# Performance work log

Hardware: AMD Instinct MI355X
Metric: run time of the kernel (lower is better)

## Reference

```python
import jax, jax.numpy as jnp
import numpy as np

N_NODES = 100000


def setup_inputs() -> dict:
    key = jax.random.key(0)
    k1, k2, k3, k4, k5 = jax.random.split(key, 5)
    dim_in, dim_out = 128, 128
    x = jax.random.normal(k1, (N_NODES, dim_in), dtype=jnp.float32)
    edge_index = jax.random.randint(k2, (2, 1600000), 0, N_NODES, dtype=jnp.int64)
    # PyG SAGEConv params: lin_l (neighbor path, with bias), lin_r (root path, no bias)
    s = 1.0 / np.sqrt(dim_in)
    W_l = jax.random.uniform(k3, (dim_in, dim_out), jnp.float32, -s, s)
    b_l = jax.random.uniform(k4, (dim_out,), jnp.float32, -s, s)
    W_r = jax.random.uniform(k5, (dim_in, dim_out), jnp.float32, -s, s)
    return {"x": x, "edge_index": edge_index, "W_l": W_l, "b_l": b_l, "W_r": W_r}


def reference(x, edge_index, W_l, b_l, W_r):
    src, dst = edge_index[0], edge_index[1]
    # mean aggregation of source features onto target nodes
    gathered = x[src]                                   # [E, d_in]
    summed = jax.ops.segment_sum(gathered, dst, num_segments=N_NODES)
    ones = jnp.ones((edge_index.shape[1],), dtype=x.dtype)
    count = jax.ops.segment_sum(ones, dst, num_segments=N_NODES)
    agg = summed / jnp.maximum(count, 1.0)[:, None]     # [N, d_in]
    # out = lin_l(agg) + lin_r(x)
    return agg @ W_l + b_l + x @ W_r
```

## Files before the change

kernel.cpp:

```cpp
#include <hip/hip_runtime.h>

#define N_NODES 100000
#define DIM 128
#define NE 1600000
#define NTILES (N_NODES / 8)
#define GEMM_BLOCKS 2048
#define CHUNK 512
#define NCHUNK ((N_NODES + CHUNK - 1) / CHUNK)
#define NBKT2 2048
#define NB64 ((N_NODES + 63) / 64)
#define NBLK_BIN 200
#define EPB (NE / NBLK_BIN)
#define BK_CAP 2048

typedef unsigned short u16;
typedef __attribute__((ext_vector_type(8))) short bf16x8;
typedef __attribute__((ext_vector_type(4))) float f32x4;

__device__ __forceinline__ float bf2f(u16 h) {
  return __uint_as_float(((unsigned int)h) << 16);
}
__device__ __forceinline__ u16 f2bf(float f) {
  unsigned int u = __float_as_uint(f);
  unsigned int lsb = (u >> 16) & 1u;
  u += 0x7fffu + lsb;
  return (u16)(u >> 16);
}


__global__ __launch_bounds__(256) void convert_k(const float* __restrict__ x,
                                                 u16* __restrict__ A) {
  int t = blockIdx.x * 256 + threadIdx.x;
  int row = t >> 5;
  int c = (t & 31) * 4;
  float4 v = *(const float4*)(x + (size_t)row * DIM + c);
  ushort4 o;
  o.x = f2bf(v.x); o.y = f2bf(v.y); o.z = f2bf(v.z); o.w = f2bf(v.w);
  *(ushort4*)(A + (size_t)row * 256 + c) = o;
}

__global__ __launch_bounds__(256) void hist2048_k(const int* __restrict__ ei,
                                                  int* __restrict__ gh) {
  __shared__ int h[NBKT2];
  for (int i = threadIdx.x; i < NBKT2; i += 256) h[i] = 0;
  __syncthreads();
  int e0 = blockIdx.x * EPB;
  for (int i = threadIdx.x; i < EPB; i += 256)
    atomicAdd(&h[ei[NE + e0 + i] >> 6], 1);
  __syncthreads();
  for (int i = threadIdx.x; i < NBKT2; i += 256)
    if (h[i]) atomicAdd(&gh[i], h[i]);
}

__global__ __launch_bounds__(1024) void scan2048_k(const int* __restrict__ gh,
                                                   int* __restrict__ base,
                                                   int* __restrict__ cur) {
  __shared__ int p[1024];
  int t = threadIdx.x;
  int a = gh[2 * t], b = gh[2 * t + 1];
  p[t] = a + b;
  __syncthreads();
  for (int off = 1; off < 1024; off <<= 1) {
    int add = (t >= off) ? p[t - off] : 0;
    __syncthreads();
    p[t] += add;
    __syncthreads();
  }
  int e0 = p[t] - (a + b);
  base[2 * t] = e0;       cur[2 * t] = e0;
  base[2 * t + 1] = e0 + a; cur[2 * t + 1] = e0 + a;
  if (t == 1023) base[NBKT2] = p[t];
}

__global__ __launch_bounds__(256) void scatter_bin_k(const int* __restrict__ ei,
                                                     int* __restrict__ cur,
                                                     int* __restrict__ binned) {
  __shared__ int h[NBKT2];
  __shared__ int bbase[NBKT2];
  for (int i = threadIdx.x; i < NBKT2; i += 256) h[i] = 0;
  __syncthreads();
  int e0 = blockIdx.x * EPB;
  for (int i = threadIdx.x; i < EPB; i += 256)
    atomicAdd(&h[ei[NE + e0 + i] >> 6], 1);
  __syncthreads();
  for (int i = threadIdx.x; i < NBKT2; i += 256) {
    int c = h[i];
    bbase[i] = c ? atomicAdd(&cur[i], c) : 0;
    h[i] = 0;
  }
  __syncthreads();
  for (int i = threadIdx.x; i < EPB; i += 256) {
    int src = ei[e0 + i];
    int dst = ei[NE + e0 + i];
    int b = dst >> 6;
    int l = atomicAdd(&h[b], 1);
    binned[bbase[b] + l] = ((dst & 63) << 17) | src;
  }
}

__global__ __launch_bounds__(256) void aggB_k(const int* __restrict__ base,
                                              const int* __restrict__ binned,
                                              u16* __restrict__ A) {
  __shared__ int srcS[BK_CAP];
  __shared__ int hist[64];
  __shared__ int off[64];
  __shared__ int cur[64];
  const int b = blockIdx.x;
  const int lo = base[b];
  int cnt = base[b + 1] - lo;
  if (cnt > BK_CAP) cnt = BK_CAP;

  if (threadIdx.x < 64) hist[threadIdx.x] = 0;
  __syncthreads();
  for (int i = threadIdx.x; i < cnt; i += 256)
    atomicAdd(&hist[binned[lo + i] >> 17], 1);
  __syncthreads();
  if (threadIdx.x < 64) off[threadIdx.x] = hist[threadIdx.x];
  __syncthreads();
  for (int st = 1; st < 64; st <<= 1) {
    int add = 0;
    if (threadIdx.x < 64 && threadIdx.x >= st) add = off[threadIdx.x - st];
    __syncthreads();
    if (threadIdx.x < 64) off[threadIdx.x] += add;
    __syncthreads();
  }
  if (threadIdx.x < 64) cur[threadIdx.x] = off[threadIdx.x] - hist[threadIdx.x];
  __syncthreads();
  for (int i = threadIdx.x; i < cnt; i += 256) {
    int rec = binned[lo + i];
    int l = atomicAdd(&cur[rec >> 17], 1);
    srcS[l] = rec & 0x1FFFF;
  }
  __syncthreads();

  const int wid = threadIdx.x >> 6;
  const int lane = threadIdx.x & 63;
  const int node0 = b * 64;
  for (int ln = wid; ln < 64; ln += 4) {
    int node = node0 + ln;
    if (node >= N_NODES) break;
    int d = hist[ln];
    int e1 = off[ln];
    int j = e1 - d;
    float ax = 0.f, ay = 0.f;
    for (; j + 4 <= e1; j += 4) {
      int s0 = srcS[j], s1 = srcS[j + 1], s2 = srcS[j + 2], s3 = srcS[j + 3];
      unsigned u0 = *(const unsigned*)(A + (size_t)s0 * 256 + lane * 2);
      unsigned u1 = *(const unsigned*)(A + (size_t)s1 * 256 + lane * 2);
      unsigned u2 = *(const unsigned*)(A + (size_t)s2 * 256 + lane * 2);
      unsigned u3 = *(const unsigned*)(A + (size_t)s3 * 256 + lane * 2);
      ax += bf2f((u16)u0) + bf2f((u16)u1) + bf2f((u16)u2) + bf2f((u16)u3);
      ay += bf2f((u16)(u0 >> 16)) + bf2f((u16)(u1 >> 16)) +
            bf2f((u16)(u2 >> 16)) + bf2f((u16)(u3 >> 16));
    }
    for (; j < e1; ++j) {
      unsigned u0 = *(const unsigned*)(A + (size_t)srcS[j] * 256 + lane * 2);
      ax += bf2f((u16)u0);
      ay += bf2f((u16)(u0 >> 16));
    }
    float scale = 1.0f / fmaxf((float)d, 1.0f);
    unsigned p = (unsigned)f2bf(ax * scale) | ((unsigned)f2bf(ay * scale) << 16);
    *(unsigned*)(A + (size_t)node * 256 + 128 + lane * 2) = p;
  }
}

__global__ __launch_bounds__(256) void wt_k(const float* __restrict__ Wl,
                                            const float* __restrict__ Wr,
                                            u16* __restrict__ Wt) {
  int n = blockIdx.x;
  int k = threadIdx.x;
  float v = (k < 128) ? Wr[(size_t)k * DIM + n] : Wl[(size_t)(k - 128) * DIM + n];
  Wt[(size_t)n * 256 + k] = f2bf(v);
}

__global__ __launch_bounds__(256) void gemm_mfma(const u16* __restrict__ A,
                                                 const u16* __restrict__ Wt,
                                                 const float* __restrict__ bias,
                                                 float* __restrict__ out) {
  const int wave = threadIdx.x >> 6;
  const int lane = threadIdx.x & 63;
  const int m = lane & 15;
  const int q = lane >> 4;
  const int n0 = wave * 32;

  bf16x8 Bf[2][8];
#pragma unroll
  for (int t = 0; t < 2; ++t) {
    const u16* bp = Wt + (size_t)(n0 + t * 16 + m) * 256 + q * 8;
#pragma unroll
    for (int s = 0; s < 8; ++s) Bf[t][s] = *(const bf16x8*)(bp + s * 32);
  }
  const float b0 = bias[n0 + m];
  const float b1 = bias[n0 + 16 + m];

  for (int rt = blockIdx.x; rt < N_NODES / 16; rt += gridDim.x) {
    const int row0 = rt * 16;
    const u16* ap = A + (size_t)(row0 + m) * 256 + q * 8;
    bf16x8 Af[8];
#pragma unroll
    for (int s = 0; s < 8; ++s) Af[s] = *(const bf16x8*)(ap + s * 32);
    f32x4 acc0 = {0.f, 0.f, 0.f, 0.f};
    f32x4 acc1 = {0.f, 0.f, 0.f, 0.f};
#pragma unroll
    for (int s = 0; s < 8; ++s) {
      acc0 = __builtin_amdgcn_mfma_f32_16x16x32_bf16(Af[s], Bf[0][s], acc0, 0, 0, 0);
      acc1 = __builtin_amdgcn_mfma_f32_16x16x32_bf16(Af[s], Bf[1][s], acc1, 0, 0, 0);
    }
    float* o = out + (size_t)(row0 + q * 4) * DIM + n0 + m;
#pragma unroll
    for (int r = 0; r < 4; ++r) {
      o[(size_t)r * DIM] = acc0[r] + b0;
      o[(size_t)r * DIM + 16] = acc1[r] + b1;
    }
  }
}

__global__ __launch_bounds__(256) void hist_k(const int* __restrict__ ei,
                                              int* __restrict__ deg) {
  int e = blockIdx.x * 256 + threadIdx.x;
  if (e < NE) atomicAdd(&deg[ei[NE + e]], 1);
}

__global__ __launch_bounds__(512) void scan_sum_k(const int* __restrict__ deg,
                                                  int* __restrict__ partials) {
  __shared__ int s[CHUNK];
  int i = blockIdx.x * CHUNK + threadIdx.x;
  s[threadIdx.x] = (i < N_NODES) ? deg[i] : 0;
  __syncthreads();
  for (int off = 256; off > 0; off >>= 1) {
    if (threadIdx.x < off) s[threadIdx.x] += s[threadIdx.x + off];
    __syncthreads();
  }
  if (threadIdx.x == 0) partials[blockIdx.x] = s[0];
}

__global__ __launch_bounds__(256) void scan_part_k(int* __restrict__ partials) {
  __shared__ int s[256];
  int t = threadIdx.x;
  int v = (t < NCHUNK) ? partials[t] : 0;
  s[t] = v;
  __syncthreads();
  for (int off = 1; off < 256; off <<= 1) {
    int add = (t >= off) ? s[t - off] : 0;
    __syncthreads();
    s[t] += add;
    __syncthreads();
  }
  if (t < NCHUNK) partials[t] = s[t] - v;
}

__global__ __launch_bounds__(512) void scan_out_k(const int* __restrict__ deg,
                                                  const int* __restrict__ partials,
                                                  int* __restrict__ offsets,
                                                  int* __restrict__ cursor) {
  __shared__ int s[CHUNK];
  int t = threadIdx.x;
  int i = blockIdx.x * CHUNK + t;
  int v = (i < N_NODES) ? deg[i] : 0;
  s[t] = v;
  __syncthreads();
  for (int off = 1; off < CHUNK; off <<= 1) {
    int add = (t >= off) ? s[t - off] : 0;
    __syncthreads();
    s[t] += add;
    __syncthreads();
  }
  if (i < N_NODES) {
    int excl = partials[blockIdx.x] + s[t] - v;
    offsets[i] = excl;
    cursor[i] = excl;
  }
  if (i == 0) offsets[N_NODES] = NE;
}

__global__ __launch_bounds__(256) void fill_k(const int* __restrict__ ei,
                                              int* __restrict__ cursor,
                                              int* __restrict__ csr) {
  int e = blockIdx.x * 256 + threadIdx.x;
  if (e < NE) {
    int dst = ei[NE + e];
    int pos = atomicAdd(&cursor[dst], 1);
    csr[pos] = ei[e];
  }
}

__global__ __launch_bounds__(256) void agg_f32_k(const int* __restrict__ offsets,
                                                 const int* __restrict__ csr,
                                                 const float* __restrict__ x,
                                                 float* __restrict__ agg) {
  int node = blockIdx.x * 4 + (threadIdx.x >> 6);
  int lane = threadIdx.x & 63;
  int beg = offsets[node], end = offsets[node + 1];
  float ax = 0.f, ay = 0.f;
  int i = beg;
  for (; i + 4 <= end; i += 4) {
    int s0 = csr[i], s1 = csr[i + 1], s2 = csr[i + 2], s3 = csr[i + 3];
    float2 v0 = *(const float2*)(x + (size_t)s0 * DIM + lane * 2);
    float2 v1 = *(const float2*)(x + (size_t)s1 * DIM + lane * 2);
    float2 v2 = *(const float2*)(x + (size_t)s2 * DIM + lane * 2);
    float2 v3 = *(const float2*)(x + (size_t)s3 * DIM + lane * 2);
    ax += v0.x + v1.x + v2.x + v3.x;
    ay += v0.y + v1.y + v2.y + v3.y;
  }
  for (; i < end; ++i) {
    float2 v0 = *(const float2*)(x + (size_t)csr[i] * DIM + lane * 2);
    ax += v0.x;
    ay += v0.y;
  }
  float scale = 1.0f / fmaxf((float)(end - beg), 1.0f);
  float2 r;
  r.x = ax * scale;
  r.y = ay * scale;
  *(float2*)(agg + (size_t)node * DIM + lane * 2) = r;
}

__global__ __launch_bounds__(256) void gemm_xw(const float* __restrict__ x,
                                               const float* __restrict__ W,
                                               const float* __restrict__ b,
                                               float* __restrict__ out) {
  __shared__ float Ws[DIM * DIM];
  for (int i = threadIdx.x; i < DIM * DIM; i += 256) Ws[i] = W[i];
  __syncthreads();
  const int c = threadIdx.x & 127;
  const int half = threadIdx.x >> 7;
  const float bias = b[c];
  for (int tile = blockIdx.x; tile < NTILES; tile += gridDim.x) {
    const int row0 = tile * 8 + half * 4;
    const float* r = x + (size_t)row0 * DIM;
    float a0 = 0.f, a1 = 0.f, a2 = 0.f, a3 = 0.f;
#pragma unroll 8
    for (int k4 = 0; k4 < 32; ++k4) {
      float4 p0 = *(const float4*)(r + 0 * DIM + k4 * 4);
      float4 p1 = *(const float4*)(r + 1 * DIM + k4 * 4);
      float4 p2 = *(const float4*)(r + 2 * DIM + k4 * 4);
      float4 p3 = *(const float4*)(r + 3 * DIM + k4 * 4);
      const float* wp = &Ws[k4 * 4 * DIM + c];
      float w0 = wp[0 * DIM], w1 = wp[1 * DIM], w2 = wp[2 * DIM], w3 = wp[3 * DIM];
      a0 += p0.x * w0 + p0.y * w1 + p0.z * w2 + p0.w * w3;
      a1 += p1.x * w0 + p1.y * w1 + p1.z * w2 + p1.w * w3;
      a2 += p2.x * w0 + p2.y * w1 + p2.z * w2 + p2.w * w3;
      a3 += p3.x * w0 + p3.y * w1 + p3.z * w2 + p3.w * w3;
    }
    out[(size_t)(row0 + 0) * DIM + c] = a0 + bias;
    out[(size_t)(row0 + 1) * DIM + c] = a1 + bias;
    out[(size_t)(row0 + 2) * DIM + c] = a2 + bias;
    out[(size_t)(row0 + 3) * DIM + c] = a3 + bias;
  }
}

__global__ __launch_bounds__(256) void gemm_aw(const float* __restrict__ agg,
                                               const float* __restrict__ W,
                                               float* __restrict__ out) {
  __shared__ float Ws[DIM * DIM];
  for (int i = threadIdx.x; i < DIM * DIM; i += 256) Ws[i] = W[i];
  __syncthreads();
  const int c = threadIdx.x & 127;
  const int half = threadIdx.x >> 7;
  for (int tile = blockIdx.x; tile < NTILES; tile += gridDim.x) {
    const int row0 = tile * 8 + half * 4;
    const float* r = agg + (size_t)row0 * DIM;
    float a0 = 0.f, a1 = 0.f, a2 = 0.f, a3 = 0.f;
#pragma unroll 8
    for (int k4 = 0; k4 < 32; ++k4) {
      float4 p0 = *(const float4*)(r + 0 * DIM + k4 * 4);
      float4 p1 = *(const float4*)(r + 1 * DIM + k4 * 4);
      float4 p2 = *(const float4*)(r + 2 * DIM + k4 * 4);
      float4 p3 = *(const float4*)(r + 3 * DIM + k4 * 4);
      const float* wp = &Ws[k4 * 4 * DIM + c];
      float w0 = wp[0 * DIM], w1 = wp[1 * DIM], w2 = wp[2 * DIM], w3 = wp[3 * DIM];
      a0 += p0.x * w0 + p0.y * w1 + p0.z * w2 + p0.w * w3;
      a1 += p1.x * w0 + p1.y * w1 + p1.z * w2 + p1.w * w3;
      a2 += p2.x * w0 + p2.y * w1 + p2.z * w2 + p2.w * w3;
      a3 += p3.x * w0 + p3.y * w1 + p3.z * w2 + p3.w * w3;
    }
    out[(size_t)(row0 + 0) * DIM + c] += a0;
    out[(size_t)(row0 + 1) * DIM + c] += a1;
    out[(size_t)(row0 + 2) * DIM + c] += a2;
    out[(size_t)(row0 + 3) * DIM + c] += a3;
  }
}

extern "C" void kernel_launch(void* const* d_in, const int* in_sizes, int n_in,
                              void* d_out, int out_size, void* d_ws, size_t ws_size,
                              hipStream_t stream) {
  const float* x  = (const float*)d_in[0];
  const int*   ei = (const int*)d_in[1];
  const float* Wl = (const float*)d_in[2];
  const float* bl = (const float*)d_in[3];
  const float* Wr = (const float*)d_in[4];
  float* out = (float*)d_out;

  u16* A        = (u16*)d_ws;
  u16* Wt       = A + (size_t)N_NODES * 256;
  int* binned   = (int*)(Wt + 128 * 256);
  int* bktHist  = binned + NE;
  int* bktBase  = bktHist + NBKT2;
  int* bktCur   = bktBase + NBKT2 + 1;
  size_t needed = (size_t)N_NODES * 512 + 65536 + (size_t)NE * 4 +
                  (NBKT2 + NBKT2 + 1 + NBKT2) * 4;

  if (ws_size >= needed) {
    hipMemsetAsync(bktHist, 0, NBKT2 * sizeof(int), stream);
    hipLaunchKernelGGL(convert_k, dim3(12500), dim3(256), 0, stream, x, A);
    hipLaunchKernelGGL(hist2048_k, dim3(NBLK_BIN), dim3(256), 0, stream, ei, bktHist);
    hipLaunchKernelGGL(scan2048_k, dim3(1), dim3(1024), 0, stream,
                       bktHist, bktBase, bktCur);
    hipLaunchKernelGGL(scatter_bin_k, dim3(NBLK_BIN), dim3(256), 0, stream,
                       ei, bktCur, binned);
    hipLaunchKernelGGL(aggB_k, dim3(NB64), dim3(256), 0, stream,
                       bktBase, binned, A);
    hipLaunchKernelGGL(wt_k, dim3(128), dim3(256), 0, stream, Wl, Wr, Wt);
    hipLaunchKernelGGL(gemm_mfma, dim3(1280), dim3(256), 0, stream,
                       A, Wt, bl, out);
  } else {
    int* deg2      = (int*)d_ws;
    int* offsets2  = deg2 + N_NODES;
    int* partials2 = offsets2 + 100004;
    int* csr2      = partials2 + 256;
    float* agg     = (float*)(csr2 + NE);
    hipMemsetAsync(deg2, 0, (size_t)N_NODES * sizeof(int), stream);
    hipLaunchKernelGGL(hist_k, dim3((NE + 255) / 256), dim3(256), 0, stream, ei, deg2);
    hipLaunchKernelGGL(scan_sum_k, dim3(NCHUNK), dim3(CHUNK), 0, stream, deg2, partials2);
    hipLaunchKernelGGL(scan_part_k, dim3(1), dim3(256), 0, stream, partials2);
    hipLaunchKernelGGL(scan_out_k, dim3(NCHUNK), dim3(CHUNK), 0, stream,
                       deg2, partials2, offsets2, deg2);
    hipLaunchKernelGGL(fill_k, dim3((NE + 255) / 256), dim3(256), 0, stream,
                       ei, deg2, csr2);
    hipLaunchKernelGGL(agg_f32_k, dim3(N_NODES / 4), dim3(256), 0, stream,
                       offsets2, csr2, x, agg);
    hipLaunchKernelGGL(gemm_xw, dim3(GEMM_BLOCKS), dim3(256), 0, stream,
                       x, Wr, bl, out);
    hipLaunchKernelGGL(gemm_aw, dim3(GEMM_BLOCKS), dim3(256), 0, stream,
                       agg, Wl, out);
  }
}
```

Before: 270.8 us.

## Fuse convert with histogram, scan with weight transpose; split A; prefetch GEMM tiles

Merges the bf16 conversion with the destination histogram and the bucket scan with the weight transpose, which removes two kernel launches. Buckets shrink to 32 nodes (4096 buckets) so there are more aggregation blocks with less shared memory each, and aggregation caches binned records in shared memory instead of reading them twice. The bf16 x copy and the aggregated features now live in two separate dense 128-wide arrays instead of one interleaved 256-wide array, which makes gathers denser. The GEMM now software-prefetches the next row tile and uses 1250 blocks. Risks: a 32-node bucket that overflows the 1024-entry cap is silently truncated, and the 12500-block fused kernel carries a 16 KB shared array in every block.

```diff
diff --git a/kernel.cpp b/kernel.cpp
--- a/kernel.cpp
+++ b/kernel.cpp
@@ -7,11 +7,11 @@
 #define GEMM_BLOCKS 2048
 #define CHUNK 512
 #define NCHUNK ((N_NODES + CHUNK - 1) / CHUNK)
-#define NBKT2 2048
-#define NB64 ((N_NODES + 63) / 64)
+#define NBKT 4096
+#define NB32 (N_NODES / 32)
 #define NBLK_BIN 200
 #define EPB (NE / NBLK_BIN)
-#define BK_CAP 2048
+#define BK_CAP 1024
 
 typedef unsigned short u16;
 typedef __attribute__((ext_vector_type(8))) short bf16x8;
@@ -28,62 +28,77 @@
 }
 
 
-__global__ __launch_bounds__(256) void convert_k(const float* __restrict__ x,
-                                                 u16* __restrict__ A) {
+__global__ __launch_bounds__(256) void convert_hist_k(const float* __restrict__ x,
+                                                      const int* __restrict__ ei,
+                                                      u16* __restrict__ Ax,
+                                                      int* __restrict__ gh) {
+  __shared__ int h[NBKT];
   int t = blockIdx.x * 256 + threadIdx.x;
   int row = t >> 5;
   int c = (t & 31) * 4;
   float4 v = *(const float4*)(x + (size_t)row * DIM + c);
   ushort4 o;
   o.x = f2bf(v.x); o.y = f2bf(v.y); o.z = f2bf(v.z); o.w = f2bf(v.w);
-  *(ushort4*)(A + (size_t)row * 256 + c) = o;
-}
-
-__global__ __launch_bounds__(256) void hist2048_k(const int* __restrict__ ei,
-                                                  int* __restrict__ gh) {
-  __shared__ int h[NBKT2];
-  for (int i = threadIdx.x; i < NBKT2; i += 256) h[i] = 0;
-  __syncthreads();
-  int e0 = blockIdx.x * EPB;
-  for (int i = threadIdx.x; i < EPB; i += 256)
-    atomicAdd(&h[ei[NE + e0 + i] >> 6], 1);
-  __syncthreads();
-  for (int i = threadIdx.x; i < NBKT2; i += 256)
-    if (h[i]) atomicAdd(&gh[i], h[i]);
-}
-
-__global__ __launch_bounds__(1024) void scan2048_k(const int* __restrict__ gh,
-                                                   int* __restrict__ base,
-                                                   int* __restrict__ cur) {
+  *(ushort4*)(Ax + (size_t)row * DIM + c) = o;
+
+  if (blockIdx.x < NBLK_BIN) {
+    for (int i = threadIdx.x; i < NBKT; i += 256) h[i] = 0;
+    __syncthreads();
+    int e0 = blockIdx.x * EPB;
+    for (int i = threadIdx.x; i < EPB; i += 256)
+      atomicAdd(&h[ei[NE + e0 + i] >> 5], 1);
+    __syncthreads();
+    for (int i = threadIdx.x; i < NBKT; i += 256)
+      if (h[i]) atomicAdd(&gh[i], h[i]);
+  }
+}
+
+__global__ __launch_bounds__(1024) void scan_wt_k(const int* __restrict__ gh,
+                                                  int* __restrict__ base,
+                                                  int* __restrict__ cur,
+                                                  const float* __restrict__ Wl,
+                                                  const float* __restrict__ Wr,
+                                                  u16* __restrict__ Wt) {
   __shared__ int p[1024];
-  int t = threadIdx.x;
-  int a = gh[2 * t], b = gh[2 * t + 1];
-  p[t] = a + b;
-  __syncthreads();
-  for (int off = 1; off < 1024; off <<= 1) {
-    int add = (t >= off) ? p[t - off] : 0;
-    __syncthreads();
-    p[t] += add;
-    __syncthreads();
-  }
-  int e0 = p[t] - (a + b);
-  base[2 * t] = e0;       cur[2 * t] = e0;
-  base[2 * t + 1] = e0 + a; cur[2 * t + 1] = e0 + a;
-  if (t == 1023) base[NBKT2] = p[t];
+  if (blockIdx.x == 0) {
+    int t = threadIdx.x;
+    int v0 = gh[4 * t], v1 = gh[4 * t + 1], v2 = gh[4 * t + 2], v3 = gh[4 * t + 3];
+    int s = v0 + v1 + v2 + v3;
+    p[t] = s;
+    __syncthreads();
+    for (int off = 1; off < 1024; off <<= 1) {
+      int add = (t >= off) ? p[t - off] : 0;
+      __syncthreads();
+      p[t] += add;
+      __syncthreads();
+    }
+    int e = p[t] - s;
+    base[4 * t] = e;              cur[4 * t] = e;
+    base[4 * t + 1] = e + v0;     cur[4 * t + 1] = e + v0;
+    base[4 * t + 2] = e + v0 + v1;     cur[4 * t + 2] = e + v0 + v1;
+    base[4 * t + 3] = e + v0 + v1 + v2; cur[4 * t + 3] = e + v0 + v1 + v2;
+    if (t == 1023) base[NBKT] = p[t];
+  } else {
+    int idx = (blockIdx.x - 1) * 1024 + threadIdx.x;
+    int n = idx >> 8;
+    int k = idx & 255;
+    float v = (k < 128) ? Wr[(size_t)k * DIM + n] : Wl[(size_t)(k - 128) * DIM + n];
+    Wt[(size_t)n * 256 + k] = f2bf(v);
+  }
 }
 
 __global__ __launch_bounds__(256) void scatter_bin_k(const int* __restrict__ ei,
                                                      int* __restrict__ cur,
                                                      int* __restrict__ binned) {
-  __shared__ int h[NBKT2];
-  __shared__ int bbase[NBKT2];
-  for (int i = threadIdx.x; i < NBKT2; i += 256) h[i] = 0;
+  __shared__ int h[NBKT];
+  __shared__ int bbase[NBKT];
+  for (int i = threadIdx.x; i < NBKT; i += 256) h[i] = 0;
   __syncthreads();
   int e0 = blockIdx.x * EPB;
   for (int i = threadIdx.x; i < EPB; i += 256)
-    atomicAdd(&h[ei[NE + e0 + i] >> 6], 1);
-  __syncthreads();
-  for (int i = threadIdx.x; i < NBKT2; i += 256) {
+    atomicAdd(&h[ei[NE + e0 + i] >> 5], 1);
+  __syncthreads();
+  for (int i = threadIdx.x; i < NBKT; i += 256) {
     int c = h[i];
     bbase[i] = c ? atomicAdd(&cur[i], c) : 0;
     h[i] = 0;
@@ -92,42 +107,47 @@
   for (int i = threadIdx.x; i < EPB; i += 256) {
     int src = ei[e0 + i];
     int dst = ei[NE + e0 + i];
-    int b = dst >> 6;
+    int b = dst >> 5;
     int l = atomicAdd(&h[b], 1);
-    binned[bbase[b] + l] = ((dst & 63) << 17) | src;
+    binned[bbase[b] + l] = ((dst & 31) << 17) | src;
   }
 }
 
 __global__ __launch_bounds__(256) void aggB_k(const int* __restrict__ base,
                                               const int* __restrict__ binned,
-                                              u16* __restrict__ A) {
+                                              const u16* __restrict__ Ax,
+                                              u16* __restrict__ Ag) {
+  __shared__ int recS[BK_CAP];
   __shared__ int srcS[BK_CAP];
-  __shared__ int hist[64];
-  __shared__ int off[64];
-  __shared__ int cur[64];
+  __shared__ int hist[32];
+  __shared__ int off[32];
+  __shared__ int cur[32];
   const int b = blockIdx.x;
   const int lo = base[b];
   int cnt = base[b + 1] - lo;
   if (cnt > BK_CAP) cnt = BK_CAP;
 
-  if (threadIdx.x < 64) hist[threadIdx.x] = 0;
-  __syncthreads();
-  for (int i = threadIdx.x; i < cnt; i += 256)
-    atomicAdd(&hist[binned[lo + i] >> 17], 1);
-  __syncthreads();
-  if (threadIdx.x < 64) off[threadIdx.x] = hist[threadIdx.x];
-  __syncthreads();
-  for (int st = 1; st < 64; st <<= 1) {
-    int add = 0;
-    if (threadIdx.x < 64 && threadIdx.x >= st) add = off[threadIdx.x - st];
-    __syncthreads();
-    if (threadIdx.x < 64) off[threadIdx.x] += add;
-    __syncthreads();
-  }
-  if (threadIdx.x < 64) cur[threadIdx.x] = off[threadIdx.x] - hist[threadIdx.x];
+  if (threadIdx.x < 32) hist[threadIdx.x] = 0;
   __syncthreads();
   for (int i = threadIdx.x; i < cnt; i += 256) {
     int rec = binned[lo + i];
+    recS[i] = rec;
+    atomicAdd(&hist[rec >> 17], 1);
+  }
+  __syncthreads();
+  if (threadIdx.x < 32) off[threadIdx.x] = hist[threadIdx.x];
+  __syncthreads();
+  for (int st = 1; st < 32; st <<= 1) {
+    int add = 0;
+    if (threadIdx.x < 32 && threadIdx.x >= st) add = off[threadIdx.x - st];
+    __syncthreads();
+    if (threadIdx.x < 32) off[threadIdx.x] += add;
+    __syncthreads();
+  }
+  if (threadIdx.x < 32) cur[threadIdx.x] = off[threadIdx.x] - hist[threadIdx.x];
+  __syncthreads();
+  for (int i = threadIdx.x; i < cnt; i += 256) {
+    int rec = recS[i];
     int l = atomicAdd(&cur[rec >> 17], 1);
     srcS[l] = rec & 0x1FFFF;
   }
@@ -135,45 +155,36 @@
 
   const int wid = threadIdx.x >> 6;
   const int lane = threadIdx.x & 63;
-  const int node0 = b * 64;
-  for (int ln = wid; ln < 64; ln += 4) {
+  const int node0 = b * 32;
+  for (int ln = wid; ln < 32; ln += 4) {
     int node = node0 + ln;
-    if (node >= N_NODES) break;
     int d = hist[ln];
     int e1 = off[ln];
     int j = e1 - d;
     float ax = 0.f, ay = 0.f;
     for (; j + 4 <= e1; j += 4) {
       int s0 = srcS[j], s1 = srcS[j + 1], s2 = srcS[j + 2], s3 = srcS[j + 3];
-      unsigned u0 = *(const unsigned*)(A + (size_t)s0 * 256 + lane * 2);
-      unsigned u1 = *(const unsigned*)(A + (size_t)s1 * 256 + lane * 2);
-      unsigned u2 = *(const unsigned*)(A + (size_t)s2 * 256 + lane * 2);
-      unsigned u3 = *(const unsigned*)(A + (size_t)s3 * 256 + lane * 2);
+      unsigned u0 = *(const unsigned*)(Ax + (size_t)s0 * DIM + lane * 2);
+      unsigned u1 = *(const unsigned*)(Ax + (size_t)s1 * DIM + lane * 2);
+      unsigned u2 = *(const unsigned*)(Ax + (size_t)s2 * DIM + lane * 2);
+      unsigned u3 = *(const unsigned*)(Ax + (size_t)s3 * DIM + lane * 2);
       ax += bf2f((u16)u0) + bf2f((u16)u1) + bf2f((u16)u2) + bf2f((u16)u3);
       ay += bf2f((u16)(u0 >> 16)) + bf2f((u16)(u1 >> 16)) +
             bf2f((u16)(u2 >> 16)) + bf2f((u16)(u3 >> 16));
     }
     for (; j < e1; ++j) {
-      unsigned u0 = *(const unsigned*)(A + (size_t)srcS[j] * 256 + lane * 2);
+      unsigned u0 = *(const unsigned*)(Ax + (size_t)srcS[j] * DIM + lane * 2);
       ax += bf2f((u16)u0);
       ay += bf2f((u16)(u0 >> 16));
     }
     float scale = 1.0f / fmaxf((float)d, 1.0f);
     unsigned p = (unsigned)f2bf(ax * scale) | ((unsigned)f2bf(ay * scale) << 16);
-    *(unsigned*)(A + (size_t)node * 256 + 128 + lane * 2) = p;
-  }
-}
-
-__global__ __launch_bounds__(256) void wt_k(const float* __restrict__ Wl,
-                                            const float* __restrict__ Wr,
-                                            u16* __restrict__ Wt) {
-  int n = blockIdx.x;
-  int k = threadIdx.x;
-  float v = (k < 128) ? Wr[(size_t)k * DIM + n] : Wl[(size_t)(k - 128) * DIM + n];
-  Wt[(size_t)n * 256 + k] = f2bf(v);
-}
-
-__global__ __launch_bounds__(256) void gemm_mfma(const u16* __restrict__ A,
+    *(unsigned*)(Ag + (size_t)node * DIM + lane * 2) = p;
+  }
+}
+
+__global__ __launch_bounds__(256) void gemm_mfma(const u16* __restrict__ Ax,
+                                                 const u16* __restrict__ Ag,
                                                  const u16* __restrict__ Wt,
                                                  const float* __restrict__ bias,
                                                  float* __restrict__ out) {
@@ -193,25 +204,45 @@
   const float b0 = bias[n0 + m];
   const float b1 = bias[n0 + 16 + m];
 
-  for (int rt = blockIdx.x; rt < N_NODES / 16; rt += gridDim.x) {
-    const int row0 = rt * 16;
-    const u16* ap = A + (size_t)(row0 + m) * 256 + q * 8;
-    bf16x8 Af[8];
-#pragma unroll
-    for (int s = 0; s < 8; ++s) Af[s] = *(const bf16x8*)(ap + s * 32);
+  const int NT = N_NODES / 16;
+  int rt = blockIdx.x;
+  bf16x8 Ac[8];
+  {
+    const u16* apx = Ax + (size_t)(rt * 16 + m) * DIM + q * 8;
+    const u16* apg = Ag + (size_t)(rt * 16 + m) * DIM + q * 8;
+#pragma unroll
+    for (int s = 0; s < 4; ++s) Ac[s] = *(const bf16x8*)(apx + s * 32);
+#pragma unroll
+    for (int s = 4; s < 8; ++s) Ac[s] = *(const bf16x8*)(apg + (s - 4) * 32);
+  }
+  while (true) {
+    int rn = rt + gridDim.x;
+    bf16x8 An[8];
+    if (rn < NT) {
+      const u16* apx = Ax + (size_t)(rn * 16 + m) * DIM + q * 8;
+      const u16* apg = Ag + (size_t)(rn * 16 + m) * DIM + q * 8;
+#pragma unroll
+      for (int s = 0; s < 4; ++s) An[s] = *(const bf16x8*)(apx + s * 32);
+#pragma unroll
+      for (int s = 4; s < 8; ++s) An[s] = *(const bf16x8*)(apg + (s - 4) * 32);
+    }
     f32x4 acc0 = {0.f, 0.f, 0.f, 0.f};
     f32x4 acc1 = {0.f, 0.f, 0.f, 0.f};
 #pragma unroll
     for (int s = 0; s < 8; ++s) {
-      acc0 = __builtin_amdgcn_mfma_f32_16x16x32_bf16(Af[s], Bf[0][s], acc0, 0, 0, 0);
-      acc1 = __builtin_amdgcn_mfma_f32_16x16x32_bf16(Af[s], Bf[1][s], acc1, 0, 0, 0);
-    }
-    float* o = out + (size_t)(row0 + q * 4) * DIM + n0 + m;
+      acc0 = __builtin_amdgcn_mfma_f32_16x16x32_bf16(Ac[s], Bf[0][s], acc0, 0, 0, 0);
+      acc1 = __builtin_amdgcn_mfma_f32_16x16x32_bf16(Ac[s], Bf[1][s], acc1, 0, 0, 0);
+    }
+    float* o = out + (size_t)(rt * 16 + q * 4) * DIM + n0 + m;
 #pragma unroll
     for (int r = 0; r < 4; ++r) {
       o[(size_t)r * DIM] = acc0[r] + b0;
       o[(size_t)r * DIM + 16] = acc1[r] + b1;
     }
+    if (rn >= NT) break;
+#pragma unroll
+    for (int s = 0; s < 8; ++s) Ac[s] = An[s];
+    rt = rn;
   }
 }
 
@@ -390,28 +421,28 @@
   const float* Wr = (const float*)d_in[4];
   float* out = (float*)d_out;
 
-  u16* A        = (u16*)d_ws;
-  u16* Wt       = A + (size_t)N_NODES * 256;
+  u16* Ax       = (u16*)d_ws;
+  u16* Ag       = Ax + (size_t)N_NODES * DIM;
+  u16* Wt       = Ag + (size_t)N_NODES * DIM;
   int* binned   = (int*)(Wt + 128 * 256);
   int* bktHist  = binned + NE;
-  int* bktBase  = bktHist + NBKT2;
-  int* bktCur   = bktBase + NBKT2 + 1;
-  size_t needed = (size_t)N_NODES * 512 + 65536 + (size_t)NE * 4 +
-                  (NBKT2 + NBKT2 + 1 + NBKT2) * 4;
+  int* bktBase  = bktHist + NBKT;
+  int* bktCur   = bktBase + NBKT + 1;
+  size_t needed = (size_t)N_NODES * DIM * 2 * 2 + 65536 + (size_t)NE * 4 +
+                  (NBKT + NBKT + 1 + NBKT) * 4;
 
   if (ws_size >= needed) {
-    hipMemsetAsync(bktHist, 0, NBKT2 * sizeof(int), stream);
-    hipLaunchKernelGGL(convert_k, dim3(12500), dim3(256), 0, stream, x, A);
-    hipLaunchKernelGGL(hist2048_k, dim3(NBLK_BIN), dim3(256), 0, stream, ei, bktHist);
-    hipLaunchKernelGGL(scan2048_k, dim3(1), dim3(1024), 0, stream,
-                       bktHist, bktBase, bktCur);
+    hipMemsetAsync(bktHist, 0, NBKT * sizeof(int), stream);
+    hipLaunchKernelGGL(convert_hist_k, dim3(12500), dim3(256), 0, stream,
+                       x, ei, Ax, bktHist);
+    hipLaunchKernelGGL(scan_wt_k, dim3(33), dim3(1024), 0, stream,
+                       bktHist, bktBase, bktCur, Wl, Wr, Wt);
     hipLaunchKernelGGL(scatter_bin_k, dim3(NBLK_BIN), dim3(256), 0, stream,
                        ei, bktCur, binned);
-    hipLaunchKernelGGL(aggB_k, dim3(NB64), dim3(256), 0, stream,
-                       bktBase, binned, A);
-    hipLaunchKernelGGL(wt_k, dim3(128), dim3(256), 0, stream, Wl, Wr, Wt);
-    hipLaunchKernelGGL(gemm_mfma, dim3(1280), dim3(256), 0, stream,
-                       A, Wt, bl, out);
+    hipLaunchKernelGGL(aggB_k, dim3(NB32), dim3(256), 0, stream,
+                       bktBase, binned, Ax, Ag);
+    hipLaunchKernelGGL(gemm_mfma, dim3(1250), dim3(256), 0, stream,
+                       Ax, Ag, Wt, bl, out);
   } else {
     int* deg2      = (int*)d_ws;
     int* offsets2  = deg2 + N_NODES;
```

New measurement: 266.0 us. About the same (-1.8%).
